# Performance work log

Hardware: AMD Instinct MI355X
Metric: run time of the kernel (lower is better)

## Reference

```python
import jax, jax.numpy as jnp
import numpy as np

DT = 0.002  # hardcoded dt0 in SDE.__call__
B, T, D = 4096, 2500, 3


def setup_inputs() -> dict:
    key = jax.random.key(0)
    ks = jax.random.split(key, 6)
    # drift/diffusion scaled by 0.1 so 2500-step Euler paths stay numerically stable in fp32
    return {
        "x0": jax.random.normal(ks[0], (B, D), jnp.float32),
        "drift": jax.random.normal(ks[1], (D, D), jnp.float32) * 0.1,
        "drift_bias": jax.random.normal(ks[2], (D,), jnp.float32),
        "diffusion": jax.random.normal(ks[3], (D, D), jnp.float32) * 0.1,
        "diffusion_bias": jax.random.normal(ks[4], (D,), jnp.float32) * 0.1,
        # standard-normal Brownian increments (scaled by sqrt(dt) inside reference)
        "noise": jax.random.normal(ks[5], (T, B, D), jnp.float32),
    }


def reference(x0, drift, drift_bias, diffusion, diffusion_bias, noise):
    # Euler-Maruyama: x_{k+1} = x_k + (A x_k + b) dt + diag(C x_k + d) dW_k
    # (diag(v) @ dW == v * dW elementwise), vmapped over batch via broadcasting.
    dt = jnp.asarray(DT, x0.dtype)
    sqrt_dt = jnp.sqrt(dt)

    def step(x, eps):
        dW = sqrt_dt * eps                       # [B, D]
        x_new = x + (x @ drift.T + drift_bias) * dt \
                + (x @ diffusion.T + diffusion_bias) * dW
        return x_new, x_new

    _, ys = jax.lax.scan(step, x0, noise)        # ys: [T, B, D]
    paths = jnp.concatenate([x0[None], ys], axis=0)  # [T+1, B, D], SaveAt includes t0
    return jnp.transpose(paths, (1, 0, 2))       # [B, T+1, D] like vmapped sol.ys
```

## Files before the change

kernel.cpp:

```cpp
#include <hip/hip_runtime.h>
#include <math.h>
#include <type_traits>


constexpr int B_N  = 4096;
constexpr int T_N  = 2500;
constexpr int CL   = 64;
constexpr int NFC  = T_N / CL;
constexpr int NCH  = NFC + 1;
constexpr int FLP  = 8;
constexpr int ROWF = (T_N + 1) * 3;

template <int N> using ic = std::integral_constant<int, N>;
typedef float f4v __attribute__((ext_vector_type(4)));


__global__ __launch_bounds__(64)
void sde_chunk_transforms(const float* __restrict__ A,
                          const float* __restrict__ bv,
                          const float* __restrict__ C,
                          const float* __restrict__ dv,
                          const float* __restrict__ noise,
                          float* __restrict__ trans)
{
    const int b = blockIdx.x * 64 + threadIdx.x;
    const int c = blockIdx.y;

    const float dt  = 0.002f;
    const float sdt = sqrtf(dt);

    float IA[3][3], Cs[3][3], bdt[3], ds[3];
#pragma unroll
    for (int i = 0; i < 3; ++i) {
        bdt[i] = bv[i] * dt;
        ds[i]  = dv[i] * sdt;
#pragma unroll
        for (int j = 0; j < 3; ++j) {
            IA[i][j] = A[i * 3 + j] * dt + (i == j ? 1.0f : 0.0f);
            Cs[i][j] = C[i * 3 + j] * sdt;
        }
    }

    float M[3][3] = {{1,0,0},{0,1,0},{0,0,1}};
    float v[3] = {0, 0, 0};

    const float* __restrict__ nb = noise + (size_t)c * CL * (B_N * 3) + (size_t)b * 3;
    const size_t nstride = (size_t)B_N * 3;

    float bufA[FLP][3], bufB[FLP][3];

    auto loadChunk = [&](float (&buf)[FLP][3], int s) {
#pragma unroll
        for (int k = 0; k < FLP; ++k) {
            const float* p = nb + ((size_t)s * FLP + k) * nstride;
            buf[k][0] = p[0];
            buf[k][1] = p[1];
            buf[k][2] = p[2];
        }
    };

    auto compChunk = [&](const float (&buf)[FLP][3]) {
#pragma unroll
        for (int k = 0; k < FLP; ++k) {
            const float e[3] = { buf[k][0], buf[k][1], buf[k][2] };
            float S[3][3], t[3];
#pragma unroll
            for (int i = 0; i < 3; ++i) {
                t[i] = fmaf(e[i], ds[i], bdt[i]);
#pragma unroll
                for (int j = 0; j < 3; ++j)
                    S[i][j] = fmaf(e[i], Cs[i][j], IA[i][j]);
            }
            float nM[3][3], nv[3];
#pragma unroll
            for (int i = 0; i < 3; ++i) {
#pragma unroll
                for (int j = 0; j < 3; ++j)
                    nM[i][j] = fmaf(S[i][2], M[2][j], fmaf(S[i][1], M[1][j], S[i][0] * M[0][j]));
                nv[i] = fmaf(S[i][2], v[2], fmaf(S[i][1], v[1], S[i][0] * v[0])) + t[i];
            }
#pragma unroll
            for (int i = 0; i < 3; ++i) {
                v[i] = nv[i];
#pragma unroll
                for (int j = 0; j < 3; ++j) M[i][j] = nM[i][j];
            }
        }
    };

    loadChunk(bufA, 0);
    loadChunk(bufB, 1);
    compChunk(bufA); loadChunk(bufA, 2);
    compChunk(bufB); loadChunk(bufB, 3);
    compChunk(bufA); loadChunk(bufA, 4);
    compChunk(bufB); loadChunk(bufB, 5);
    compChunk(bufA); loadChunk(bufA, 6);
    compChunk(bufB); loadChunk(bufB, 7);
    compChunk(bufA);
    compChunk(bufB);

    float* tp = trans + ((size_t)c * B_N + b) * 12;
    float4 w0 = { M[0][0], M[0][1], M[0][2], M[1][0] };
    float4 w1 = { M[1][1], M[1][2], M[2][0], M[2][1] };
    float4 w2 = { M[2][2], v[0],    v[1],    v[2]    };
    ((float4*)tp)[0] = w0;
    ((float4*)tp)[1] = w1;
    ((float4*)tp)[2] = w2;
}

__global__ __launch_bounds__(64)
void sde_scan(const float* __restrict__ x0,
              float* __restrict__ trans)
{
    const int b = blockIdx.x * 64 + threadIdx.x;

    float x[3] = { x0[b * 3 + 0], x0[b * 3 + 1], x0[b * 3 + 2] };

    float4* tp0 = (float4*)(trans + (size_t)b * 12);
    const size_t cs = (size_t)B_N * 3;

    float4 qa0, qa1, qa2, qb0, qb1, qb2, qc0, qc1, qc2, qd0, qd1, qd2;

    auto L = [&](int s, float4& r0, float4& r1, float4& r2) {
        const float4* tn = tp0 + (size_t)s * cs;
        r0 = tn[0]; r1 = tn[1]; r2 = tn[2];
    };
    auto useSlot = [&](int s, const float4& a0, const float4& a1, const float4& a2) {
        tp0[(size_t)s * cs] = make_float4(x[0], x[1], x[2], 0.0f);
        const float n0 = fmaf(a0.x, x[0], fmaf(a0.y, x[1], fmaf(a0.z, x[2], a2.y)));
        const float n1 = fmaf(a0.w, x[0], fmaf(a1.x, x[1], fmaf(a1.y, x[2], a2.z)));
        const float n2 = fmaf(a1.z, x[0], fmaf(a1.w, x[1], fmaf(a2.x, x[2], a2.w)));
        x[0] = n0; x[1] = n1; x[2] = n2;
    };

    L(0, qa0, qa1, qa2);
    L(1, qb0, qb1, qb2);
    L(2, qc0, qc1, qc2);
    L(3, qd0, qd1, qd2);

    for (int it = 0; it < 9; ++it) {
        const int s = it * 4;
        useSlot(s + 0, qa0, qa1, qa2);
        if (s + 4 < NFC) L(s + 4, qa0, qa1, qa2);
        useSlot(s + 1, qb0, qb1, qb2);
        if (s + 5 < NFC) L(s + 5, qb0, qb1, qb2);
        useSlot(s + 2, qc0, qc1, qc2);
        if (s + 6 < NFC) L(s + 6, qc0, qc1, qc2);
        useSlot(s + 3, qd0, qd1, qd2);
        if (s + 7 < NFC) L(s + 7, qd0, qd1, qd2);
    }
    useSlot(36, qa0, qa1, qa2);
    useSlot(37, qb0, qb1, qb2);
    useSlot(38, qc0, qc1, qc2);

    tp0[(size_t)NFC * cs] = make_float4(x[0], x[1], x[2], 0.0f);
}

__global__ __launch_bounds__(64)
void sde_replay(const float* __restrict__ A,
                const float* __restrict__ bv,
                const float* __restrict__ C,
                const float* __restrict__ dv,
                const float* __restrict__ noise,
                const float* __restrict__ trans,
                float* __restrict__ out)
{
    __shared__ float tile[96][66];

    const int lane = threadIdx.x & 63;
    const int pg   = blockIdx.x & 63;
    const int c    = (NCH - 1) - (blockIdx.x >> 6);
    const int b    = (pg << 6) | lane;
    const int phi  = (11 * lane) & 15;

    const float dt  = 0.002f;
    const float sdt = sqrtf(dt);

    float Adt[3][3], Cs[3][3], bdt[3], dsv[3];
#pragma unroll
    for (int i = 0; i < 3; ++i) {
        bdt[i] = bv[i] * dt;
        dsv[i] = dv[i] * sdt;
#pragma unroll
        for (int j = 0; j < 3; ++j) {
            Adt[i][j] = A[i * 3 + j] * dt;
            Cs[i][j]  = C[i * 3 + j] * sdt;
        }
    }

    const f4v xb = __builtin_nontemporal_load(
        (const f4v*)(trans + ((size_t)c * B_N + b) * 12));
    float x0r = xb.x, x1r = xb.y, x2r = xb.z;

    const float* __restrict__ nb0 = noise + (size_t)b * 3;
    const size_t nstride = (size_t)B_N * 3;
    const int base = c * CL;

    auto stepf = [&](float e0, float e1, float e2) {
        const float a0 = fmaf(Adt[0][2], x2r, fmaf(Adt[0][1], x1r, fmaf(Adt[0][0], x0r, bdt[0])));
        const float a1 = fmaf(Adt[1][2], x2r, fmaf(Adt[1][1], x1r, fmaf(Adt[1][0], x0r, bdt[1])));
        const float a2 = fmaf(Adt[2][2], x2r, fmaf(Adt[2][1], x1r, fmaf(Adt[2][0], x0r, bdt[2])));

        const float c0 = fmaf(Cs[0][2], x2r, fmaf(Cs[0][1], x1r, fmaf(Cs[0][0], x0r, dsv[0])));
        const float c1 = fmaf(Cs[1][2], x2r, fmaf(Cs[1][1], x1r, fmaf(Cs[1][0], x0r, dsv[1])));
        const float c2 = fmaf(Cs[2][2], x2r, fmaf(Cs[2][1], x1r, fmaf(Cs[2][0], x0r, dsv[2])));

        x0r = fmaf(c0, e0, x0r + a0);
        x1r = fmaf(c1, e1, x1r + a1);
        x2r = fmaf(c2, e2, x2r + a2);
    };

    if (c == NFC) {
        float* op = out + (size_t)b * ROWF;
        if (phi == 0) {
            op[2496 * 3 + 0] = x0r; op[2496 * 3 + 1] = x1r; op[2496 * 3 + 2] = x2r;
        }
#pragma unroll
        for (int k = 0; k < 4; ++k) {
            const float* p = nb0 + (size_t)(2496 + k) * nstride;
            stepf(p[0], p[1], p[2]);
            const int j = k + 1;
            if (j >= phi) {
                float* d = op + (size_t)(2496 + j) * 3;
                d[0] = x0r; d[1] = x1r; d[2] = x2r;
            }
        }
        return;
    }

    const bool c0   = (c == 0);
    const bool last = (c == NFC - 1);

    auto tileWrite = [&](int j) {
        const int r = (j & 31) * 3;
        tile[r + 0][lane] = x0r;
        tile[r + 1][lane] = x1r;
        tile[r + 2][lane] = x2r;
    };

    auto rawGuard = [&]() {
        asm volatile("s_waitcnt lgkmcnt(0)" ::: "memory");
        __builtin_amdgcn_sched_barrier(0);
    };
    auto warGuard = [&]() {
        asm volatile("s_waitcnt lgkmcnt(0)" ::: "memory");
        __builtin_amdgcn_sched_barrier(0);
    };

    const int h   = lane >> 4;
    const int m   = lane & 15;
    const int phh = (11 * h) & 15;
    float* const outG = out + (size_t)(pg << 6) * ROWF + (size_t)base * 3;

    auto flush = [&](auto fc, bool maskTail) {
        constexpr int F = decltype(fc)::value;
        rawGuard();
#pragma unroll
        for (int i = 0; i < 16; ++i) {
            const int P    = 4 * i + h;
            const int phiP = (12 * i + phh) & 15;
            const int j    = phiP + 16 * F + m;
            const int r    = (j & 31) * 3;
            const float v0 = tile[r + 0][P];
            const float v1 = tile[r + 1][P];
            const float v2 = tile[r + 2][P];
            if (!maskTail || (phiP + m) <= 20) {
                float* d = outG + (size_t)P * ROWF + (size_t)j * 3;
                __builtin_nontemporal_store(v0, d + 0);
                __builtin_nontemporal_store(v1, d + 1);
                __builtin_nontemporal_store(v2, d + 2);
            }
        }
    };

    float bufA[16][3], bufB[16][3];
    auto loadN = [&](float (&buf)[16][3], int kbase, auto cnt) {
        constexpr int CNT = decltype(cnt)::value;
#pragma unroll
        for (int k = 0; k < CNT; ++k) {
            int g = base + kbase + k;
            g = g > (T_N - 1) ? (T_N - 1) : g;
            const float* p = nb0 + (size_t)g * nstride;
            buf[k][0] = p[0];
            buf[k][1] = p[1];
            buf[k][2] = p[2];
        }
    };

    loadN(bufA, 0,  ic<16>{});
    loadN(bufB, 16, ic<16>{});

    tileWrite(0);
    if (c0 && phi > 0) {
        float* d = outG + (size_t)lane * ROWF;
        d[0] = x0r; d[1] = x1r; d[2] = x2r;
    }

#pragma unroll
    for (int k = 0; k < 16; ++k) {
        stepf(bufA[k][0], bufA[k][1], bufA[k][2]);
        tileWrite(k + 1);
        if (c0 && (k + 1) < phi) {
            float* d = outG + (size_t)lane * ROWF + (size_t)(k + 1) * 3;
            d[0] = x0r; d[1] = x1r; d[2] = x2r;
        }
    }
    loadN(bufA, 32, ic<16>{});

#pragma unroll
    for (int k = 0; k < 15; ++k) {
        stepf(bufB[k][0], bufB[k][1], bufB[k][2]);
        tileWrite(k + 17);
    }

    flush(ic<0>{}, false);

    warGuard();
    stepf(bufB[15][0], bufB[15][1], bufB[15][2]);
    tileWrite(32);
    loadN(bufB, 48, ic<16>{});
#pragma unroll
    for (int k = 0; k < 15; ++k) {
        stepf(bufA[k][0], bufA[k][1], bufA[k][2]);
        tileWrite(33 + k);
    }

    flush(ic<1>{}, false);

    warGuard();
    stepf(bufA[15][0], bufA[15][1], bufA[15][2]);
    tileWrite(48);
    loadN(bufA, 64, ic<15>{});
#pragma unroll
    for (int k = 0; k < 15; ++k) {
        stepf(bufB[k][0], bufB[k][1], bufB[k][2]);
        tileWrite(49 + k);
    }

    flush(ic<2>{}, false);

    warGuard();
    stepf(bufB[15][0], bufB[15][1], bufB[15][2]);
    tileWrite(64);
#pragma unroll
    for (int k = 0; k < 15; ++k) {
        stepf(bufA[k][0], bufA[k][1], bufA[k][2]);
        tileWrite(65 + k);
    }

    flush(ic<3>{}, last);
}

extern "C" void kernel_launch(void* const* d_in, const int* in_sizes, int n_in,
                              void* d_out, int out_size, void* d_ws, size_t ws_size,
                              hipStream_t stream) {
    const float* x0    = (const float*)d_in[0];
    const float* A     = (const float*)d_in[1];
    const float* bv    = (const float*)d_in[2];
    const float* C     = (const float*)d_in[3];
    const float* dv    = (const float*)d_in[4];
    const float* noise = (const float*)d_in[5];
    float* out = (float*)d_out;

    float* trans = (float*)d_ws;

    dim3 gridPC(B_N / 64, NFC);

    sde_chunk_transforms<<<gridPC, 64, 0, stream>>>(A, bv, C, dv, noise, trans);
    sde_scan<<<B_N / 64, 64, 0, stream>>>(x0, trans);
    sde_replay<<<64 * NCH, 64, 0, stream>>>(A, bv, C, dv, noise, trans, out);
}
```

Before: 80.81 us.

## Replace LDS-transposed output flush with direct per-thread stores in replay

Drops the shared-memory tile transpose and coalesced nontemporal flush in the replay kernel, so each thread writes its own path steps straight to global memory inside a windowed range. The noise prefetch changes from 16-step to 8-step double buffers, and chunk order is now forward instead of reversed. This removes the LDS traffic and waitcnt barriers but gives up coalescing: each lane writes 12-byte records with a stride of a whole row, which costs more write transactions.

```diff
diff --git a/kernel.cpp b/kernel.cpp
--- a/kernel.cpp
+++ b/kernel.cpp
@@ -165,11 +165,9 @@
                 const float* __restrict__ trans,
                 float* __restrict__ out)
 {
-    __shared__ float tile[96][66];
-
     const int lane = threadIdx.x & 63;
     const int pg   = blockIdx.x & 63;
-    const int c    = (NCH - 1) - (blockIdx.x >> 6);
+    const int c    = blockIdx.x >> 6;
     const int b    = (pg << 6) | lane;
     const int phi  = (11 * lane) & 15;
 
@@ -230,54 +228,20 @@
 
     const bool c0   = (c == 0);
     const bool last = (c == NFC - 1);
-
-    auto tileWrite = [&](int j) {
-        const int r = (j & 31) * 3;
-        tile[r + 0][lane] = x0r;
-        tile[r + 1][lane] = x1r;
-        tile[r + 2][lane] = x2r;
-    };
-
-    auto rawGuard = [&]() {
-        asm volatile("s_waitcnt lgkmcnt(0)" ::: "memory");
-        __builtin_amdgcn_sched_barrier(0);
-    };
-    auto warGuard = [&]() {
-        asm volatile("s_waitcnt lgkmcnt(0)" ::: "memory");
-        __builtin_amdgcn_sched_barrier(0);
-    };
-
-    const int h   = lane >> 4;
-    const int m   = lane & 15;
-    const int phh = (11 * h) & 15;
-    float* const outG = out + (size_t)(pg << 6) * ROWF + (size_t)base * 3;
-
-    auto flush = [&](auto fc, bool maskTail) {
-        constexpr int F = decltype(fc)::value;
-        rawGuard();
-#pragma unroll
-        for (int i = 0; i < 16; ++i) {
-            const int P    = 4 * i + h;
-            const int phiP = (12 * i + phh) & 15;
-            const int j    = phiP + 16 * F + m;
-            const int r    = (j & 31) * 3;
-            const float v0 = tile[r + 0][P];
-            const float v1 = tile[r + 1][P];
-            const float v2 = tile[r + 2][P];
-            if (!maskTail || (phiP + m) <= 20) {
-                float* d = outG + (size_t)P * ROWF + (size_t)j * 3;
-                __builtin_nontemporal_store(v0, d + 0);
-                __builtin_nontemporal_store(v1, d + 1);
-                __builtin_nontemporal_store(v2, d + 2);
-            }
-        }
-    };
-
-    float bufA[16][3], bufB[16][3];
-    auto loadN = [&](float (&buf)[16][3], int kbase, auto cnt) {
-        constexpr int CNT = decltype(cnt)::value;
-#pragma unroll
-        for (int k = 0; k < CNT; ++k) {
+    const int  jlo  = c0 ? 0 : phi;
+    const int  jhi1 = phi + 64;
+    const int  jhi2 = last ? (T_N + 1 - base) : 127;
+    const int  jhi  = jhi1 < jhi2 ? jhi1 : jhi2;
+
+    float* const op = out + (size_t)b * ROWF + (size_t)base * 3;
+
+    if (jlo == 0) { op[0] = x0r; op[1] = x1r; op[2] = x2r; }
+
+    float bufA[FLP][3], bufB[FLP][3];
+
+    auto loadN = [&](float (&buf)[FLP][3], int kbase) {
+#pragma unroll
+        for (int k = 0; k < FLP; ++k) {
             int g = base + kbase + k;
             g = g > (T_N - 1) ? (T_N - 1) : g;
             const float* p = nb0 + (size_t)g * nstride;
@@ -287,68 +251,30 @@
         }
     };
 
-    loadN(bufA, 0,  ic<16>{});
-    loadN(bufB, 16, ic<16>{});
-
-    tileWrite(0);
-    if (c0 && phi > 0) {
-        float* d = outG + (size_t)lane * ROWF;
-        d[0] = x0r; d[1] = x1r; d[2] = x2r;
-    }
-
-#pragma unroll
-    for (int k = 0; k < 16; ++k) {
-        stepf(bufA[k][0], bufA[k][1], bufA[k][2]);
-        tileWrite(k + 1);
-        if (c0 && (k + 1) < phi) {
-            float* d = outG + (size_t)lane * ROWF + (size_t)(k + 1) * 3;
-            d[0] = x0r; d[1] = x1r; d[2] = x2r;
-        }
-    }
-    loadN(bufA, 32, ic<16>{});
-
-#pragma unroll
-    for (int k = 0; k < 15; ++k) {
-        stepf(bufB[k][0], bufB[k][1], bufB[k][2]);
-        tileWrite(k + 17);
-    }
-
-    flush(ic<0>{}, false);
-
-    warGuard();
-    stepf(bufB[15][0], bufB[15][1], bufB[15][2]);
-    tileWrite(32);
-    loadN(bufB, 48, ic<16>{});
-#pragma unroll
-    for (int k = 0; k < 15; ++k) {
-        stepf(bufA[k][0], bufA[k][1], bufA[k][2]);
-        tileWrite(33 + k);
-    }
-
-    flush(ic<1>{}, false);
-
-    warGuard();
-    stepf(bufA[15][0], bufA[15][1], bufA[15][2]);
-    tileWrite(48);
-    loadN(bufA, 64, ic<15>{});
-#pragma unroll
-    for (int k = 0; k < 15; ++k) {
-        stepf(bufB[k][0], bufB[k][1], bufB[k][2]);
-        tileWrite(49 + k);
-    }
-
-    flush(ic<2>{}, false);
-
-    warGuard();
-    stepf(bufB[15][0], bufB[15][1], bufB[15][2]);
-    tileWrite(64);
-#pragma unroll
-    for (int k = 0; k < 15; ++k) {
-        stepf(bufA[k][0], bufA[k][1], bufA[k][2]);
-        tileWrite(65 + k);
-    }
-
-    flush(ic<3>{}, last);
+    auto compGroup = [&](const float (&buf)[FLP][3], int jbase) {
+#pragma unroll
+        for (int k = 0; k < FLP; ++k) {
+            stepf(buf[k][0], buf[k][1], buf[k][2]);
+            const int j = jbase + k + 1;
+            if (j >= jlo && j < jhi) {
+                float* d = op + (size_t)j * 3;
+                d[0] = x0r; d[1] = x1r; d[2] = x2r;
+            }
+        }
+    };
+
+    loadN(bufA, 0);
+    loadN(bufB, 8);
+    compGroup(bufA, 0);  loadN(bufA, 16);
+    compGroup(bufB, 8);  loadN(bufB, 24);
+    compGroup(bufA, 16); loadN(bufA, 32);
+    compGroup(bufB, 24); loadN(bufB, 40);
+    compGroup(bufA, 32); loadN(bufA, 48);
+    compGroup(bufB, 40); loadN(bufB, 56);
+    compGroup(bufA, 48); loadN(bufA, 64);
+    compGroup(bufB, 56); loadN(bufB, 72);
+    compGroup(bufA, 64);
+    compGroup(bufB, 72);
 }
 
 extern "C" void kernel_launch(void* const* d_in, const int* in_sizes, int n_in,
```

New measurement: 99.22 us. 1.23x slower.
